# Kernel optimization log

Hardware: AMD Instinct MI355X
Metric: run time of the kernel (lower is better)

Reference implementation:

```python
import jax, jax.numpy as jnp
import numpy as np

DIM = 1024
HEADS = 8
LN_EPS = 1e-5


def _next_fast_len(n):
    # smallest 5-smooth integer >= n (matches scipy.fftpack.next_fast_len)
    while True:
        m = n
        for p in (2, 3, 5):
            while m % p == 0:
                m //= p
        if m == 1:
            return n
        n += 1


def setup_inputs() -> dict:
    key = jax.random.key(0)
    k1, k2, k3 = jax.random.split(key, 3)
    x = jax.random.normal(k1, (4, 8192, DIM), dtype=jnp.float32)
    gamma = jnp.ones((DIM,), dtype=jnp.float32)
    beta = jnp.zeros((DIM,), dtype=jnp.float32)
    alphas = jax.random.normal(k2, (HEADS,), dtype=jnp.float32)
    param_D = jax.random.normal(k3, (DIM,), dtype=jnp.float32)
    return {"x": x, "gamma": gamma, "beta": beta, "alphas": alphas, "param_D": param_D}


def reference(x, gamma, beta, alphas, param_D):
    b, L, dim = x.shape
    h = HEADS
    # LayerNorm
    mean = jnp.mean(x, axis=-1, keepdims=True)
    var = jnp.mean((x - mean) ** 2, axis=-1, keepdims=True)
    u = (x - mean) * jax.lax.rsqrt(var + LN_EPS) * gamma + beta
    residual = u * param_D
    # per-head EMA kernel K[l, h] = a_h * (1 - a_h)^(L-1-l)
    a = jax.nn.sigmoid(alphas)  # [h]
    rev_pow = jnp.arange(L - 1, -1, -1, dtype=x.dtype)  # [L]
    K = a * (1.0 - a) ** rev_pow[:, None]  # [L, h]
    # FFT causal correlation along the sequence axis
    u4 = u.reshape(b, L, h, dim // h)  # [b, L, h, d]
    fast_len = _next_fast_len(2 * L - 1)
    f_x = jnp.fft.rfft(u4, n=fast_len, axis=1)          # [b, F, h, d]
    f_w = jnp.fft.rfft(K, n=fast_len, axis=0)           # [F, h]
    f_out = f_x * jnp.conj(f_w)[None, :, :, None]
    out = jnp.fft.irfft(f_out, n=fast_len, axis=1)      # [b, fast_len, h, d]
    out = jnp.roll(out, -1, axis=1)[:, fast_len - L: fast_len]  # [b, L, h, d]
    out = out.reshape(b, L, dim)
    return out + residual
```

## Files before the change

### kernel.cpp

```cpp
#include <hip/hip_runtime.h>
#include <math.h>

#define B 4
#define SEQ 8192
#define DIM 1024
#define HEADS 8
#define NCHUNK 128
#define CLEN (SEQ / NCHUNK)
#define LN_EPS 1e-5f

__global__ void __launch_bounds__(256) pass1_kernel(
        const float* __restrict__ x,
        const float* __restrict__ gamma,
        const float* __restrict__ beta,
        const float* __restrict__ alphas,
        float2* __restrict__ stats,
        float4* __restrict__ carry) {
    const int bid   = blockIdx.x;
    const int chunk = bid & (NCHUNK - 1);
    const int b     = bid >> 7;
    const int t     = threadIdx.x;
    const int c     = t * 4;
    const int h     = c >> 7;
    const int wave  = t >> 6;
    const int lane  = t & 63;

    const float a = 1.f / (1.f + expf(-alphas[h]));
    const float r = 1.f - a;
    const float4 g  = *(const float4*)(gamma + c);
    const float4 be = *(const float4*)(beta + c);

    __shared__ float red[2][8];

    const int rowbase = b * SEQ + chunk * CLEN;
    const float4* xp = (const float4*)x + (long)rowbase * (DIM / 4) + t;

    float4 y = make_float4(0.f, 0.f, 0.f, 0.f);
    float4 xv = xp[0];

    for (int i = 0; i < CLEN; ++i) {
        const int ip = (i + 1 < CLEN) ? i + 1 : CLEN - 1;
        float4 xnext = xp[ip * (DIM / 4)];

        float s  = xv.x + xv.y + xv.z + xv.w;
        float ss = xv.x * xv.x + xv.y * xv.y + xv.z * xv.z + xv.w * xv.w;
#pragma unroll
        for (int off = 32; off > 0; off >>= 1) {
            s  += __shfl_down(s, off);
            ss += __shfl_down(ss, off);
        }
        const int par = i & 1;
        if (lane == 0) {
            red[par][wave]     = s;
            red[par][4 + wave] = ss;
        }
        __syncthreads();
        const float S    = red[par][0] + red[par][1] + red[par][2] + red[par][3];
        const float SS   = red[par][4] + red[par][5] + red[par][6] + red[par][7];
        const float mean = S * (1.f / DIM);
        const float var  = SS * (1.f / DIM) - mean * mean;
        const float rstd = rsqrtf(var + LN_EPS);
        if (t == 0) stats[rowbase + i] = make_float2(mean, rstd);

        float4 u;
        u.x = (xv.x - mean) * rstd * g.x + be.x;
        u.y = (xv.y - mean) * rstd * g.y + be.y;
        u.z = (xv.z - mean) * rstd * g.z + be.z;
        u.w = (xv.w - mean) * rstd * g.w + be.w;
        y.x = r * y.x + a * u.x;
        y.y = r * y.y + a * u.y;
        y.z = r * y.z + a * u.z;
        y.w = r * y.w + a * u.w;

        xv = xnext;
    }
    carry[(long)bid * (DIM / 4) + t] = y;
}

__global__ void carry_scan_kernel(const float* __restrict__ alphas,
                                  const float* __restrict__ carry,
                                  float* __restrict__ excl) {
    const int tid = blockIdx.x * blockDim.x + threadIdx.x;
    const int c = tid & (DIM - 1);
    const int b = tid >> 10;
    const int h = c >> 7;

    const float a = 1.f / (1.f + expf(-alphas[h]));
    const float r = 1.f - a;
    float rn = r;
#pragma unroll
    for (int q = 0; q < 6; ++q) rn = rn * rn;

    const float* cp = carry + (long)b * NCHUNK * DIM + c;
    float*       ep = excl  + (long)b * NCHUNK * DIM + c;

    float Y = 0.f;
#pragma unroll 8
    for (int k = 0; k < NCHUNK; ++k) {
        float loc = cp[(long)k * DIM];
        ep[(long)k * DIM] = Y;
        Y = rn * Y + loc;
    }
}

__global__ void __launch_bounds__(256) pass2_kernel(
        const float* __restrict__ x,
        const float2* __restrict__ stats,
        const float* __restrict__ gamma,
        const float* __restrict__ beta,
        const float* __restrict__ alphas,
        const float* __restrict__ paramD,
        const float4* __restrict__ excl,
        float4* __restrict__ out) {
    const int bid   = blockIdx.x;
    const int chunk = bid & (NCHUNK - 1);
    const int b     = bid >> 7;
    const int t     = threadIdx.x;
    const int c     = t * 4;
    const int h     = c >> 7;

    const float a = 1.f / (1.f + expf(-alphas[h]));
    const float r = 1.f - a;
    const float4 g  = *(const float4*)(gamma  + c);
    const float4 be = *(const float4*)(beta   + c);
    const float4 D  = *(const float4*)(paramD + c);

    const int rowbase = b * SEQ + chunk * CLEN;
    const float4* xp = (const float4*)x + (long)rowbase * (DIM / 4) + t;
    float4*       op = (float4*)out     + (long)rowbase * (DIM / 4) + t;

    float4 y = excl[(long)bid * (DIM / 4) + t];

#pragma unroll 4
    for (int i = 0; i < CLEN; ++i) {
        const float2 st = stats[rowbase + i];
        float4 xv = xp[i * (DIM / 4)];
        float4 u, o;
        u.x = (xv.x - st.x) * st.y * g.x + be.x;
        u.y = (xv.y - st.x) * st.y * g.y + be.y;
        u.z = (xv.z - st.x) * st.y * g.z + be.z;
        u.w = (xv.w - st.x) * st.y * g.w + be.w;
        y.x = r * y.x + a * u.x;
        y.y = r * y.y + a * u.y;
        y.z = r * y.z + a * u.z;
        y.w = r * y.w + a * u.w;
        o.x = y.x + u.x * D.x;
        o.y = y.y + u.y * D.y;
        o.z = y.z + u.z * D.z;
        o.w = y.w + u.w * D.w;
        op[i * (DIM / 4)] = o;
    }
}

extern "C" void kernel_launch(void* const* d_in, const int* in_sizes, int n_in,
                              void* d_out, int out_size, void* d_ws, size_t ws_size,
                              hipStream_t stream) {
    const float* x      = (const float*)d_in[0];
    const float* gamma  = (const float*)d_in[1];
    const float* beta   = (const float*)d_in[2];
    const float* alphas = (const float*)d_in[3];
    const float* paramD = (const float*)d_in[4];
    float* out = (float*)d_out;

    char* ws = (char*)d_ws;
    float2* stats = (float2*)ws;
    float*  carry = (float*)(ws + (1 << 18));
    float*  excl  = (float*)(ws + (1 << 18) + (1 << 21));

    pass1_kernel<<<B * NCHUNK, 256, 0, stream>>>(
        x, gamma, beta, alphas, stats, (float4*)carry);
    carry_scan_kernel<<<B * DIM / 256, 256, 0, stream>>>(alphas, carry, excl);
    pass2_kernel<<<B * NCHUNK, 256, 0, stream>>>(
        x, stats, gamma, beta, alphas, paramD, (const float4*)excl, (float4*)out);
}
```

Before: 283.6 us.

## Double chunk count, batch LN reductions per barrier, cache stats in LDS, nontemporal stores

Chunk count rises from 128 to 256 so each pass launches twice as many blocks. Pass1 now handles four rows per barrier to cut synchronisation and shuffle latency, and prefetches four rows at a time. The carry scan is vectorised to float2 with 64-thread blocks, pass2 stages its per-row stats in shared memory, and output stores become nontemporal. The carry workspace doubles in size, and the serial scan now runs 256 steps instead of 128.

New measurement: 316.7 us. +11.7%, slower.

```diff
diff --git a/kernel.cpp b/kernel.cpp
--- a/kernel.cpp
+++ b/kernel.cpp
@@ -5,9 +5,14 @@
 #define SEQ 8192
 #define DIM 1024
 #define HEADS 8
-#define NCHUNK 128
+#define NCHUNK 256
+#define LOG_NCHUNK 8
 #define CLEN (SEQ / NCHUNK)
+#define GROUP 4
+#define NGROUP (CLEN / GROUP)
 #define LN_EPS 1e-5f
+
+typedef float vf4 __attribute__((ext_vector_type(4)));
 
 __global__ void __launch_bounds__(256) pass1_kernel(
         const float* __restrict__ x,
@@ -18,88 +23,109 @@
         float4* __restrict__ carry) {
     const int bid   = blockIdx.x;
     const int chunk = bid & (NCHUNK - 1);
-    const int b     = bid >> 7;
+    const int b     = bid >> LOG_NCHUNK;
     const int t     = threadIdx.x;
     const int c     = t * 4;
     const int h     = c >> 7;
     const int wave  = t >> 6;
     const int lane  = t & 63;
 
-    const float a = 1.f / (1.f + expf(-alphas[h]));
-    const float r = 1.f - a;
+    const float a   = 1.f / (1.f + expf(-alphas[h]));
+    const float dec = 1.f - a;
     const float4 g  = *(const float4*)(gamma + c);
     const float4 be = *(const float4*)(beta + c);
 
-    __shared__ float red[2][8];
+    __shared__ float red[2][GROUP][8];
 
     const int rowbase = b * SEQ + chunk * CLEN;
     const float4* xp = (const float4*)x + (long)rowbase * (DIM / 4) + t;
 
     float4 y = make_float4(0.f, 0.f, 0.f, 0.f);
-    float4 xv = xp[0];
-
-    for (int i = 0; i < CLEN; ++i) {
-        const int ip = (i + 1 < CLEN) ? i + 1 : CLEN - 1;
-        float4 xnext = xp[ip * (DIM / 4)];
-
-        float s  = xv.x + xv.y + xv.z + xv.w;
-        float ss = xv.x * xv.x + xv.y * xv.y + xv.z * xv.z + xv.w * xv.w;
+    float4 xv[GROUP], xn[GROUP];
+#pragma unroll
+    for (int q = 0; q < GROUP; ++q) xv[q] = xp[q * (DIM / 4)];
+
+    for (int gi = 0; gi < NGROUP; ++gi) {
+        const int nb = (gi + 1 < NGROUP) ? (gi + 1) * GROUP : gi * GROUP;
+#pragma unroll
+        for (int q = 0; q < GROUP; ++q) xn[q] = xp[(nb + q) * (DIM / 4)];
+
+        float s[GROUP], ss[GROUP];
+#pragma unroll
+        for (int q = 0; q < GROUP; ++q) {
+            s[q]  = xv[q].x + xv[q].y + xv[q].z + xv[q].w;
+            ss[q] = xv[q].x * xv[q].x + xv[q].y * xv[q].y
+                  + xv[q].z * xv[q].z + xv[q].w * xv[q].w;
+        }
 #pragma unroll
         for (int off = 32; off > 0; off >>= 1) {
-            s  += __shfl_down(s, off);
-            ss += __shfl_down(ss, off);
-        }
-        const int par = i & 1;
+#pragma unroll
+            for (int q = 0; q < GROUP; ++q) {
+                s[q]  += __shfl_down(s[q], off);
+                ss[q] += __shfl_down(ss[q], off);
+            }
+        }
+        const int par = gi & 1;
         if (lane == 0) {
-            red[par][wave]     = s;
-            red[par][4 + wave] = ss;
+#pragma unroll
+            for (int q = 0; q < GROUP; ++q) {
+                red[par][q][wave]     = s[q];
+                red[par][q][4 + wave] = ss[q];
+            }
         }
         __syncthreads();
-        const float S    = red[par][0] + red[par][1] + red[par][2] + red[par][3];
-        const float SS   = red[par][4] + red[par][5] + red[par][6] + red[par][7];
-        const float mean = S * (1.f / DIM);
-        const float var  = SS * (1.f / DIM) - mean * mean;
-        const float rstd = rsqrtf(var + LN_EPS);
-        if (t == 0) stats[rowbase + i] = make_float2(mean, rstd);
-
-        float4 u;
-        u.x = (xv.x - mean) * rstd * g.x + be.x;
-        u.y = (xv.y - mean) * rstd * g.y + be.y;
-        u.z = (xv.z - mean) * rstd * g.z + be.z;
-        u.w = (xv.w - mean) * rstd * g.w + be.w;
-        y.x = r * y.x + a * u.x;
-        y.y = r * y.y + a * u.y;
-        y.z = r * y.z + a * u.z;
-        y.w = r * y.w + a * u.w;
-
-        xv = xnext;
+#pragma unroll
+        for (int q = 0; q < GROUP; ++q) {
+            const float S    = red[par][q][0] + red[par][q][1]
+                             + red[par][q][2] + red[par][q][3];
+            const float SS   = red[par][q][4] + red[par][q][5]
+                             + red[par][q][6] + red[par][q][7];
+            const float mean = S * (1.f / DIM);
+            const float var  = SS * (1.f / DIM) - mean * mean;
+            const float rstd = rsqrtf(var + LN_EPS);
+            if (t == 0) stats[rowbase + gi * GROUP + q] = make_float2(mean, rstd);
+
+            float4 u;
+            u.x = (xv[q].x - mean) * rstd * g.x + be.x;
+            u.y = (xv[q].y - mean) * rstd * g.y + be.y;
+            u.z = (xv[q].z - mean) * rstd * g.z + be.z;
+            u.w = (xv[q].w - mean) * rstd * g.w + be.w;
+            y.x = dec * y.x + a * u.x;
+            y.y = dec * y.y + a * u.y;
+            y.z = dec * y.z + a * u.z;
+            y.w = dec * y.w + a * u.w;
+        }
+#pragma unroll
+        for (int q = 0; q < GROUP; ++q) xv[q] = xn[q];
     }
     carry[(long)bid * (DIM / 4) + t] = y;
 }
 
-__global__ void carry_scan_kernel(const float* __restrict__ alphas,
-                                  const float* __restrict__ carry,
-                                  float* __restrict__ excl) {
-    const int tid = blockIdx.x * blockDim.x + threadIdx.x;
-    const int c = tid & (DIM - 1);
-    const int b = tid >> 10;
-    const int h = c >> 7;
+__global__ void __launch_bounds__(64) carry_scan_kernel(
+        const float* __restrict__ alphas,
+        const float2* __restrict__ carry,
+        float2* __restrict__ excl) {
+    const int tid = blockIdx.x * 64 + threadIdx.x;
+    const int cc  = tid & (DIM / 2 - 1);
+    const int b   = tid >> 9;
+    const int h   = (cc * 2) >> 7;
 
     const float a = 1.f / (1.f + expf(-alphas[h]));
     const float r = 1.f - a;
     float rn = r;
 #pragma unroll
-    for (int q = 0; q < 6; ++q) rn = rn * rn;
-
-    const float* cp = carry + (long)b * NCHUNK * DIM + c;
-    float*       ep = excl  + (long)b * NCHUNK * DIM + c;
-
-    float Y = 0.f;
-#pragma unroll 8
+    for (int q = 0; q < 5; ++q) rn = rn * rn;
+
+    const float2* cp = carry + (long)b * NCHUNK * (DIM / 2) + cc;
+    float2*       ep = excl  + (long)b * NCHUNK * (DIM / 2) + cc;
+
+    float2 Y = make_float2(0.f, 0.f);
+#pragma unroll 16
     for (int k = 0; k < NCHUNK; ++k) {
-        float loc = cp[(long)k * DIM];
-        ep[(long)k * DIM] = Y;
-        Y = rn * Y + loc;
+        const float2 loc = cp[(long)k * (DIM / 2)];
+        ep[(long)k * (DIM / 2)] = Y;
+        Y.x = rn * Y.x + loc.x;
+        Y.y = rn * Y.y + loc.y;
     }
 }
 
@@ -114,13 +140,13 @@
         float4* __restrict__ out) {
     const int bid   = blockIdx.x;
     const int chunk = bid & (NCHUNK - 1);
-    const int b     = bid >> 7;
+    const int b     = bid >> LOG_NCHUNK;
     const int t     = threadIdx.x;
     const int c     = t * 4;
     const int h     = c >> 7;
 
-    const float a = 1.f / (1.f + expf(-alphas[h]));
-    const float r = 1.f - a;
+    const float a   = 1.f / (1.f + expf(-alphas[h]));
+    const float dec = 1.f - a;
     const float4 g  = *(const float4*)(gamma  + c);
     const float4 be = *(const float4*)(beta   + c);
     const float4 D  = *(const float4*)(paramD + c);
@@ -129,26 +155,31 @@
     const float4* xp = (const float4*)x + (long)rowbase * (DIM / 4) + t;
     float4*       op = (float4*)out     + (long)rowbase * (DIM / 4) + t;
 
+    __shared__ float2 strow[CLEN];
+    if (t < CLEN) strow[t] = stats[rowbase + t];
+
     float4 y = excl[(long)bid * (DIM / 4) + t];
-
-#pragma unroll 4
+    __syncthreads();
+
+#pragma unroll 8
     for (int i = 0; i < CLEN; ++i) {
-        const float2 st = stats[rowbase + i];
-        float4 xv = xp[i * (DIM / 4)];
+        const float2 st = strow[i];
+        const float4 xv = xp[i * (DIM / 4)];
         float4 u, o;
         u.x = (xv.x - st.x) * st.y * g.x + be.x;
         u.y = (xv.y - st.x) * st.y * g.y + be.y;
         u.z = (xv.z - st.x) * st.y * g.z + be.z;
         u.w = (xv.w - st.x) * st.y * g.w + be.w;
-        y.x = r * y.x + a * u.x;
-        y.y = r * y.y + a * u.y;
-        y.z = r * y.z + a * u.z;
-        y.w = r * y.w + a * u.w;
+        y.x = dec * y.x + a * u.x;
+        y.y = dec * y.y + a * u.y;
+        y.z = dec * y.z + a * u.z;
+        y.w = dec * y.w + a * u.w;
         o.x = y.x + u.x * D.x;
         o.y = y.y + u.y * D.y;
         o.z = y.z + u.z * D.z;
         o.w = y.w + u.w * D.w;
-        op[i * (DIM / 4)] = o;
+        vf4 vo = { o.x, o.y, o.z, o.w };
+        __builtin_nontemporal_store(vo, (vf4*)(op + i * (DIM / 4)));
     }
 }
 
@@ -165,11 +196,12 @@
     char* ws = (char*)d_ws;
     float2* stats = (float2*)ws;
     float*  carry = (float*)(ws + (1 << 18));
-    float*  excl  = (float*)(ws + (1 << 18) + (1 << 21));
+    float*  excl  = (float*)(ws + (1 << 18) + (1 << 22));
 
     pass1_kernel<<<B * NCHUNK, 256, 0, stream>>>(
         x, gamma, beta, alphas, stats, (float4*)carry);
-    carry_scan_kernel<<<B * DIM / 256, 256, 0, stream>>>(alphas, carry, excl);
+    carry_scan_kernel<<<B * DIM / 2 / 64, 64, 0, stream>>>(
+        alphas, (const float2*)carry, (float2*)excl);
     pass2_kernel<<<B * NCHUNK, 256, 0, stream>>>(
         x, stats, gamma, beta, alphas, paramD, (const float4*)excl, (float4*)out);
 }
```
